# Kernel optimization log

Measured on AMD Instinct MI355X. Metric: run time of the kernel, lower is better.

## Reference

```python
import jax, jax.numpy as jnp
import numpy as np

# ---- column/activation layout (matches transformer_info init kwarg) ----
N_COLS = 20          # continuous data columns
MODES = 50           # VGM modes per column (gumbel-softmax width)
SPAN = MODES + 1     # 1 tanh scalar + MODES gumbel logits
IN_DIM = 2048
OUT_DIM = N_COLS * SPAN  # 1020
TAU = 0.2
B = 16384
EPS = 1e-9

_spans = []
for i in range(N_COLS):
    st = i * SPAN
    _spans.append((st, st + 1, 0))          # tanh span (alpha)
    _spans.append((st + 1, st + SPAN, 1))   # gumbel-softmax span (beta/d)
N_SEG = len(_spans)

_seg = np.zeros(OUT_DIM, np.int32)   # segment id per output feature
_typ = np.zeros(OUT_DIM, np.int32)   # 0 = tanh, 1 = gumbel-softmax
for si, (s, e, t) in enumerate(_spans):
    _seg[s:e] = si
    _typ[s:e] = t
SEG = jnp.asarray(_seg)
TYP = jnp.asarray(_typ)


def setup_inputs() -> dict:
    key = jax.random.key(0)
    kx, kw, kb, ku = jax.random.split(key, 4)
    bound = 1.0 / np.sqrt(IN_DIM)  # init_bounded(dim=input_dim)
    x = jax.random.normal(kx, (B, IN_DIM), dtype=jnp.float32)
    W = jax.random.uniform(kw, (IN_DIM, OUT_DIM), minval=-bound, maxval=bound, dtype=jnp.float32)
    b = jax.random.uniform(kb, (OUT_DIM,), minval=-bound, maxval=bound, dtype=jnp.float32)
    u = jax.random.uniform(ku, (B, OUT_DIM), dtype=jnp.float32)  # uniform driving gumbel noise
    return {"x": x, "W": W, "b": b, "u": u}


def _segment_softmax(z):
    # softmax over each transformer_info span, fused via segment ops.
    zT = z.T  # [D, B]
    m = jax.ops.segment_max(zT, SEG, num_segments=N_SEG)      # [S, B]
    e = jnp.exp(zT - m[SEG])
    s = jax.ops.segment_sum(e, SEG, num_segments=N_SEG)       # [S, B]
    return (e / s[SEG]).T  # [B, D]


def reference(x, W, b, u):
    outputs = x @ W + b  # [B, OUT_DIM]
    # Gumbel(0,1) noise from uniform u
    g = -jnp.log(-jnp.log(jnp.clip(u, EPS, 1.0 - EPS)))
    soft = _segment_softmax((outputs + g) / TAU)
    # type 0 -> tanh, type 1 -> gumbel-softmax (single fused select)
    data_t = jnp.where(TYP == 0, jnp.tanh(outputs), soft)
    return outputs, data_t
```

## Files before the change

### kernel.cpp

```cpp
#include <hip/hip_runtime.h>
#include <stdint.h>

#define MDIM 16384
#define NDIM 1020
#define KDIM 2048
#define NPAD 1024
#define TK   (KDIM / 64)

typedef __attribute__((ext_vector_type(4))) float f32x4;
typedef __attribute__((ext_vector_type(8))) short short8;

#define MFMA16(a, b, c) __builtin_amdgcn_mfma_f32_16x16x32_bf16((a), (b), (c), 0, 0, 0)

template <int OFF>
static __device__ __forceinline__ short8 dsr(unsigned addr) {
    short8 r;
    asm volatile("ds_read_b128 %0, %1 offset:%2" : "=v"(r) : "v"(addr), "i"(OFF));
    return r;
}
template <int OFF>
static __device__ __forceinline__ void dsw64(unsigned addr, uint2 v) {
    asm volatile("ds_write_b64 %0, %1 offset:%2" :: "v"(addr), "v"(v), "i"(OFF));
}

__device__ __forceinline__ unsigned packbf(float lo, float hi) {
    const unsigned r0 = __float_as_uint(lo) + 0x8000u;
    const unsigned r1 = __float_as_uint(hi) + 0x8000u;
    return __builtin_amdgcn_perm(r1, r0, 0x07060302u);
}

__device__ __forceinline__ unsigned short f2bf(float f) {
    unsigned int u = __float_as_uint(f);
    unsigned int r = (u + 0x7FFFu + ((u >> 16) & 1u)) >> 16;
    return (unsigned short)r;
}

__global__ void prep_w_kernel(const float* __restrict__ W,
                              unsigned short* __restrict__ Wt) {
    const int id = blockIdx.x * 256 + threadIdx.x;
    const int n0 = (id & 255) * 4;
    const int k0 = (id >> 8) * 4;
    float a[4][4];
    if (n0 < NDIM) {
#pragma unroll
        for (int i = 0; i < 4; ++i) {
            const float* p = W + (size_t)(k0 + i) * NDIM + n0;
            a[i][0] = p[0]; a[i][1] = p[1]; a[i][2] = p[2]; a[i][3] = p[3];
        }
    } else {
#pragma unroll
        for (int i = 0; i < 4; ++i)
#pragma unroll
            for (int j = 0; j < 4; ++j) a[i][j] = 0.f;
    }
#pragma unroll
    for (int j = 0; j < 4; ++j) {
        uint2 p;
        p.x = (unsigned)f2bf(a[0][j]) | ((unsigned)f2bf(a[1][j]) << 16);
        p.y = (unsigned)f2bf(a[2][j]) | ((unsigned)f2bf(a[3][j]) << 16);
        *(uint2*)(Wt + (size_t)(n0 + j) * KDIM + k0) = p;
    }
}

__global__ void prep_x_kernel(const float* __restrict__ x,
                              unsigned short* __restrict__ Xb) {
    const size_t total = (size_t)MDIM * KDIM;
    const size_t stride = (size_t)gridDim.x * 256 * 8;
    for (size_t i = ((size_t)blockIdx.x * 256 + threadIdx.x) * 8; i < total; i += stride) {
        const float4 v0 = *(const float4*)(x + i);
        const float4 v1 = *(const float4*)(x + i + 4);
        uint4 p;
        p.x = (unsigned)f2bf(v0.x) | ((unsigned)f2bf(v0.y) << 16);
        p.y = (unsigned)f2bf(v0.z) | ((unsigned)f2bf(v0.w) << 16);
        p.z = (unsigned)f2bf(v1.x) | ((unsigned)f2bf(v1.y) << 16);
        p.w = (unsigned)f2bf(v1.z) | ((unsigned)f2bf(v1.w) << 16);
        *(uint4*)(Xb + i) = p;
    }
}

extern "C" __global__ __launch_bounds__(512, 2) void gemm10_kernel(
    const float* __restrict__ x,
    const unsigned short* __restrict__ Wt,
    const float* __restrict__ bias,
    float* __restrict__ out) {
    extern __shared__ unsigned short lds_raw[];

    const int tid  = threadIdx.x;
    const int lane = tid & 63;
    const int wid  = tid >> 6;
    const int wr   = wid >> 2;
    const int wc   = wid & 3;

    const int bid = blockIdx.x;
    const int swz = (bid & 7) * 32 + (bid >> 3);
    const int bm  = swz >> 2;
    const int bn  = swz & 3;

    const int srow = wid * 8 + (lane >> 3);
    const int scb  = ((lane & 7) ^ (lane >> 3)) * 8;
    const unsigned short* bS = Wt + (size_t)(bn * 256 + srow) * KDIM + scb;

#define STAGEB(BUFI, STRIPE, S) do {                                             \
    const unsigned short* sp_ =                                                  \
        bS + (size_t)((STRIPE) * 64) * KDIM + (size_t)(((S) & 31) * 64);         \
    __builtin_amdgcn_global_load_lds(                                            \
        (const __attribute__((address_space(1))) unsigned int*)sp_,              \
        (__attribute__((address_space(3))) unsigned int*)(lds_raw +              \
            (BUFI) * 32768 + 16384 + ((STRIPE) * 64 + wid * 8) * 64),            \
        16, 0, 0);                                                               \
} while (0)

    const int h = lane >> 4, g = lane & 15;
    const float* aF = x + (size_t)(bm * 256 + wid * 32 + h) * KDIM + g * 4;

    const unsigned ldsbase =
        (unsigned)(uintptr_t)(__attribute__((address_space(3))) unsigned short*)lds_raw;
    const unsigned awbE =
        ldsbase + (unsigned)(wid * 32 + h) * 128 +
        ((unsigned)((g >> 1) ^ h) << 4) + (unsigned)(g & 1) * 8;
    const unsigned awbO  = awbE ^ 0x40u;
    const unsigned awb0E = awbE,           awb0O = awbO;
    const unsigned awb1E = awbE + 65536u,  awb1O = awbO + 65536u;

    float4 av[8];
#define AGLD(T) {                                                     \
    const float* ap_ = aF + (size_t)(((T) & 31) * 64);                \
    av[0] = *(const float4*)(ap_);                                    \
    av[1] = *(const float4*)(ap_ + 4 * KDIM);                         \
    av[2] = *(const float4*)(ap_ + 8 * KDIM);                         \
    av[3] = *(const float4*)(ap_ + 12 * KDIM);                        \
    av[4] = *(const float4*)(ap_ + 16 * KDIM);                        \
    av[5] = *(const float4*)(ap_ + 20 * KDIM);                        \
    av[6] = *(const float4*)(ap_ + 24 * KDIM);                        \
    av[7] = *(const float4*)(ap_ + 28 * KDIM);                        \
}
#define CVT1(AWE, AWO, I)                                             \
    { uint2 v_;                                                       \
      v_.x = packbf(av[I].x, av[I].y);                                \
      v_.y = packbf(av[I].z, av[I].w);                                \
      dsw64<(I) * 512>(((I) & 1) ? (AWO) : (AWE), v_); }
#define CVTW(AWE, AWO)                                                \
    CVT1(AWE, AWO, 0) CVT1(AWE, AWO, 1) CVT1(AWE, AWO, 2)             \
    CVT1(AWE, AWO, 3) CVT1(AWE, AWO, 4) CVT1(AWE, AWO, 5)             \
    CVT1(AWE, AWO, 6) CVT1(AWE, AWO, 7)

    const unsigned l15 = lane & 15, hi = lane >> 4, l7 = lane & 7;
    const unsigned c0 = (unsigned)((0 * 4 + hi) ^ l7) << 4;
    const unsigned c1 = (unsigned)((1 * 4 + hi) ^ l7) << 4;
    const unsigned pbA = ldsbase + (unsigned)(wr * 128 + l15) * 128;
    const unsigned pbB = ldsbase + 32768u + (unsigned)(wc * 64 + l15) * 128;
    const unsigned aA0_0 = pbA + c0,          aA0_1 = pbA + c1;
    const unsigned aA1_0 = pbA + 65536u + c0, aA1_1 = pbA + 65536u + c1;
    const unsigned bB0_0 = pbB + c0,          bB0_1 = pbB + c1;
    const unsigned bB1_0 = pbB + 65536u + c0, bB1_1 = pbB + 65536u + c1;

    f32x4 acc[8][4];
#pragma unroll
    for (int i = 0; i < 8; ++i)
#pragma unroll
        for (int j = 0; j < 4; ++j) {
            f32x4 z = {0.f, 0.f, 0.f, 0.f};
            acc[i][j] = z;
        }

#define PH_TAIL                                                       \
    __builtin_amdgcn_s_barrier();                                     \
    asm volatile("s_waitcnt lgkmcnt(0)" ::: "memory");                \
    __builtin_amdgcn_sched_barrier(0);                                \
    __builtin_amdgcn_s_setprio(1);

#define PH_MFMA(MF0)                                                  \
    _Pragma("unroll")                                                 \
    for (int nf = 0; nf < 4; ++nf) {                                  \
        acc[MF0][nf]     = MFMA16(af0[0], bfv[nf][0], acc[MF0][nf]);      \
        acc[MF0][nf]     = MFMA16(af0[1], bfv[nf][1], acc[MF0][nf]);      \
        acc[MF0 + 1][nf] = MFMA16(af1[0], bfv[nf][0], acc[MF0 + 1][nf]);  \
        acc[MF0 + 1][nf] = MFMA16(af1[1], bfv[nf][1], acc[MF0 + 1][nf]);  \
    }                                                                 \
    __builtin_amdgcn_sched_barrier(0);                                \
    __builtin_amdgcn_s_setprio(0);

#define RDA(BUF, MF0)                                                 \
    af0[0] = dsr<(MF0) * 2048>(aA##BUF##_0);                          \
    af0[1] = dsr<(MF0) * 2048>(aA##BUF##_1);                          \
    af1[0] = dsr<(MF0) * 2048 + 2048>(aA##BUF##_0);                   \
    af1[1] = dsr<(MF0) * 2048 + 2048>(aA##BUF##_1);

#define RDB(BUF, NF)                                                  \
    bfv[NF][0] = dsr<(NF) * 2048>(bB##BUF##_0);                       \
    bfv[NF][1] = dsr<(NF) * 2048>(bB##BUF##_1);

#define TILE(T, BUF, NB, AWE, AWO)                                              \
  {                                                                             \
    short8 bfv[4][2];                                                           \
    short8 af0[2], af1[2];                                                      \
              \
    RDB(BUF, 0) RDB(BUF, 1) RDB(BUF, 2) RDB(BUF, 3)                             \
    RDA(BUF, 0)                                                                 \
    AGLD((T) + 1)                                                               \
    PH_TAIL                                                                     \
    PH_MFMA(0)                                                                  \
    __builtin_amdgcn_s_barrier();                                               \
                                                         \
    RDA(BUF, 2)                                                                 \
    STAGEB(NB, 0, (T) + 1); STAGEB(NB, 1, (T) + 1);                             \
    PH_TAIL                                                                     \
    PH_MFMA(2)                                                                  \
    __builtin_amdgcn_s_barrier();                                               \
                                                         \
    RDA(BUF, 4)                                                                 \
    STAGEB(NB, 2, (T) + 1); STAGEB(NB, 3, (T) + 1);                             \
    PH_TAIL                                                                     \
    PH_MFMA(4)                                                                  \
    __builtin_amdgcn_s_barrier();                                               \
       \
    RDA(BUF, 6)                                                                 \
    CVTW(AWE, AWO)                                                              \
    PH_TAIL                                                                     \
    PH_MFMA(6)                                                                  \
    asm volatile("s_waitcnt vmcnt(0)" ::: "memory");                            \
    __builtin_amdgcn_sched_barrier(0);                                          \
    __builtin_amdgcn_s_barrier();                                               \
  }

    AGLD(0)
    STAGEB(0, 0, 0); STAGEB(0, 1, 0); STAGEB(0, 2, 0); STAGEB(0, 3, 0);
    CVTW(awb0E, awb0O)
    asm volatile("s_waitcnt lgkmcnt(0)" ::: "memory");
    __builtin_amdgcn_sched_barrier(0);
    asm volatile("s_waitcnt vmcnt(0)" ::: "memory");
    __builtin_amdgcn_sched_barrier(0);
    __builtin_amdgcn_s_barrier();

    for (int t2 = 0; t2 < TK; t2 += 2) {
        TILE(t2,     0, 1, awb1E, awb1O)
        TILE(t2 + 1, 1, 0, awb0E, awb0O)
    }

#pragma unroll
    for (int nf = 0; nf < 4; ++nf) {
        const int col = bn * 256 + wc * 64 + nf * 16 + (lane & 15);
        if (col < NDIM) {
            const float bv = bias[col];
#pragma unroll
            for (int mf = 0; mf < 8; ++mf) {
                const int row = bm * 256 + wr * 128 + mf * 16 + ((lane >> 4) << 2);
                float* op = out + (size_t)row * NDIM + col;
#pragma unroll
                for (int r = 0; r < 4; ++r)
                    op[(size_t)r * NDIM] = acc[mf][nf][r] + bv;
            }
        }
    }
#undef STAGEB
#undef AGLD
#undef CVT1
#undef CVTW
#undef PH_TAIL
#undef PH_MFMA
#undef RDA
#undef RDB
#undef TILE
}

__global__ void gemm_bf_kernel(const unsigned short* __restrict__ Xb,
                               const unsigned short* __restrict__ Wt,
                               const float* __restrict__ bias,
                               float* __restrict__ out) {
    __shared__ __align__(16) unsigned short As[128][32];
    __shared__ __align__(16) unsigned short Bs[128][32];

    const int tid  = threadIdx.x;
    const int lane = tid & 63;
    const int wid  = tid >> 6;
    const int wr   = wid >> 1;
    const int wc   = wid & 1;
    const int bn   = blockIdx.x;
    const int bm   = blockIdx.y;

    f32x4 acc[4][4];
#pragma unroll
    for (int i = 0; i < 4; ++i)
#pragma unroll
        for (int j = 0; j < 4; ++j) {
            f32x4 z = {0.f, 0.f, 0.f, 0.f};
            acc[i][j] = z;
        }

    const unsigned short* abase =
        Xb + (size_t)(bm * 128 + wid * 16 + (lane >> 2)) * KDIM + (lane & 3) * 8;
    const unsigned short* bbase =
        Wt + (size_t)(bn * 128 + wid * 16 + (lane >> 2)) * KDIM + (lane & 3) * 8;

    for (int kt = 0; kt < KDIM; kt += 32) {
#pragma unroll
        for (int j = 0; j < 2; ++j)
            __builtin_amdgcn_global_load_lds(
                (const __attribute__((address_space(1))) unsigned int*)(abase + (size_t)j * 64 * KDIM + kt),
                (__attribute__((address_space(3))) unsigned int*)(&As[j * 64 + wid * 16][0]),
                16, 0, 0);
#pragma unroll
        for (int j = 0; j < 2; ++j)
            __builtin_amdgcn_global_load_lds(
                (const __attribute__((address_space(1))) unsigned int*)(bbase + (size_t)j * 64 * KDIM + kt),
                (__attribute__((address_space(3))) unsigned int*)(&Bs[j * 64 + wid * 16][0]),
                16, 0, 0);
        __syncthreads();

        short8 af[4], bfr[4];
#pragma unroll
        for (int mi = 0; mi < 4; ++mi)
            af[mi] = *(const short8*)&As[wr * 64 + mi * 16 + (lane & 15)][(lane >> 4) * 8];
#pragma unroll
        for (int ni = 0; ni < 4; ++ni)
            bfr[ni] = *(const short8*)&Bs[wc * 64 + ni * 16 + (lane & 15)][(lane >> 4) * 8];

#pragma unroll
        for (int mi = 0; mi < 4; ++mi)
#pragma unroll
            for (int ni = 0; ni < 4; ++ni)
                acc[mi][ni] = MFMA16(af[mi], bfr[ni], acc[mi][ni]);

        __syncthreads();
    }

#pragma unroll
    for (int ni = 0; ni < 4; ++ni) {
        const int col = bn * 128 + wc * 64 + ni * 16 + (lane & 15);
        if (col < NDIM) {
            const float bv = bias[col];
#pragma unroll
            for (int mi = 0; mi < 4; ++mi) {
                const int row = bm * 128 + wr * 64 + mi * 16 + ((lane >> 4) << 2);
                float* op = out + (size_t)row * NDIM + col;
#pragma unroll
                for (int r = 0; r < 4; ++r)
                    op[(size_t)r * NDIM] = acc[mi][ni][r] + bv;
            }
        }
    }
}

__global__ void act_kernel(const float* __restrict__ outp,
                           const float* __restrict__ u,
                           float* __restrict__ dt) {
    const int lane  = threadIdx.x & 63;
    const int gwave = (blockIdx.x * 256 + threadIdx.x) >> 6;
    const int nwave = gridDim.x * 4;
    const int total = MDIM * 20;
    const float NEG_INF = -__builtin_inff();

    for (int unit = gwave; unit < total; unit += nwave) {
        const int row = unit / 20;
        const int sp  = unit - row * 20;
        const size_t base = (size_t)row * NDIM + sp * 51;

        float o = 0.f, uu = 0.5f;
        if (lane < 51) {
            o  = outp[base + lane];
            uu = u[base + lane];
        }
        const bool soft = (lane >= 1) && (lane < 51);

        const float uc = fmaxf(uu, 1e-9f);
        const float g  = -__logf(-__logf(uc));
        float z = soft ? (o + g) * 5.0f : NEG_INF;

        float m = z;
#pragma unroll
        for (int off = 32; off; off >>= 1) m = fmaxf(m, __shfl_xor(m, off));
        float e = soft ? __expf(z - m) : 0.f;
        float s = e;
#pragma unroll
        for (int off = 32; off; off >>= 1) s += __shfl_xor(s, off);

        float res;
        if (lane == 0) {
            const float ex = __expf(-2.0f * fabsf(o));
            const float t  = (1.0f - ex) / (1.0f + ex);
            res = copysignf(t, o);
        } else {
            res = e / s;
        }
        if (lane < 51) dt[base + lane] = res;
    }
}

extern "C" void kernel_launch(void* const* d_in, const int* in_sizes, int n_in,
                              void* d_out, int out_size, void* d_ws, size_t ws_size,
                              hipStream_t stream) {
    const float* x = (const float*)d_in[0];
    const float* W = (const float*)d_in[1];
    const float* b = (const float*)d_in[2];
    const float* u = (const float*)d_in[3];
    float* out = (float*)d_out;
    float* dt  = out + (size_t)MDIM * NDIM;
    unsigned short* Wt = (unsigned short*)d_ws;
    unsigned short* Xb = Wt + (size_t)NPAD * KDIM;

    prep_w_kernel<<<512, 256, 0, stream>>>(W, Wt);

    const hipError_t attr_ok = hipFuncSetAttribute(
        (const void*)gemm10_kernel, hipFuncAttributeMaxDynamicSharedMemorySize, 131072);
    if (attr_ok == hipSuccess) {
        gemm10_kernel<<<256, 512, 131072, stream>>>(x, Wt, b, out);
    } else {
        prep_x_kernel<<<2048, 256, 0, stream>>>(x, Xb);
        gemm_bf_kernel<<<dim3(8, 128), 256, 0, stream>>>(Xb, Wt, b, out);
    }

    act_kernel<<<8192, 256, 0, stream>>>(out, u, dt);
}
```

Measured before the change: 183.4 us.

## Split GEMM block work across 16 waves with 64x64 per-wave tiles

```diff
diff --git a/kernel.cpp b/kernel.cpp
--- a/kernel.cpp
+++ b/kernel.cpp
@@ -78,7 +78,7 @@
     }
 }
 
-extern "C" __global__ __launch_bounds__(512, 2) void gemm10_kernel(
+extern "C" __global__ __launch_bounds__(1024, 4) void gemm17_kernel(
     const float* __restrict__ x,
     const unsigned short* __restrict__ Wt,
     const float* __restrict__ bias,
@@ -102,37 +102,33 @@
 
 #define STAGEB(BUFI, STRIPE, S) do {                                             \
     const unsigned short* sp_ =                                                  \
-        bS + (size_t)((STRIPE) * 64) * KDIM + (size_t)(((S) & 31) * 64);         \
+        bS + (size_t)((STRIPE) * 128) * KDIM + (size_t)(((S) & 31) * 64);        \
     __builtin_amdgcn_global_load_lds(                                            \
         (const __attribute__((address_space(1))) unsigned int*)sp_,              \
         (__attribute__((address_space(3))) unsigned int*)(lds_raw +              \
-            (BUFI) * 32768 + 16384 + ((STRIPE) * 64 + wid * 8) * 64),            \
+            (BUFI) * 32768 + 16384 + ((STRIPE) * 128 + wid * 8) * 64),           \
         16, 0, 0);                                                               \
 } while (0)
 
     const int h = lane >> 4, g = lane & 15;
-    const float* aF = x + (size_t)(bm * 256 + wid * 32 + h) * KDIM + g * 4;
+    const float* aF = x + (size_t)(bm * 256 + wid * 16 + h) * KDIM + g * 4;
 
     const unsigned ldsbase =
         (unsigned)(uintptr_t)(__attribute__((address_space(3))) unsigned short*)lds_raw;
     const unsigned awbE =
-        ldsbase + (unsigned)(wid * 32 + h) * 128 +
+        ldsbase + (unsigned)(wid * 16 + h) * 128 +
         ((unsigned)((g >> 1) ^ h) << 4) + (unsigned)(g & 1) * 8;
     const unsigned awbO  = awbE ^ 0x40u;
     const unsigned awb0E = awbE,           awb0O = awbO;
     const unsigned awb1E = awbE + 65536u,  awb1O = awbO + 65536u;
 
-    float4 av[8];
+    float4 av[4];
 #define AGLD(T) {                                                     \
     const float* ap_ = aF + (size_t)(((T) & 31) * 64);                \
     av[0] = *(const float4*)(ap_);                                    \
     av[1] = *(const float4*)(ap_ + 4 * KDIM);                         \
     av[2] = *(const float4*)(ap_ + 8 * KDIM);                         \
     av[3] = *(const float4*)(ap_ + 12 * KDIM);                        \
-    av[4] = *(const float4*)(ap_ + 16 * KDIM);                        \
-    av[5] = *(const float4*)(ap_ + 20 * KDIM);                        \
-    av[6] = *(const float4*)(ap_ + 24 * KDIM);                        \
-    av[7] = *(const float4*)(ap_ + 28 * KDIM);                        \
 }
 #define CVT1(AWE, AWO, I)                                             \
     { uint2 v_;                                                       \
@@ -140,23 +136,21 @@
       v_.y = packbf(av[I].z, av[I].w);                                \
       dsw64<(I) * 512>(((I) & 1) ? (AWO) : (AWE), v_); }
 #define CVTW(AWE, AWO)                                                \
-    CVT1(AWE, AWO, 0) CVT1(AWE, AWO, 1) CVT1(AWE, AWO, 2)             \
-    CVT1(AWE, AWO, 3) CVT1(AWE, AWO, 4) CVT1(AWE, AWO, 5)             \
-    CVT1(AWE, AWO, 6) CVT1(AWE, AWO, 7)
+    CVT1(AWE, AWO, 0) CVT1(AWE, AWO, 1) CVT1(AWE, AWO, 2) CVT1(AWE, AWO, 3)
 
     const unsigned l15 = lane & 15, hi = lane >> 4, l7 = lane & 7;
     const unsigned c0 = (unsigned)((0 * 4 + hi) ^ l7) << 4;
     const unsigned c1 = (unsigned)((1 * 4 + hi) ^ l7) << 4;
-    const unsigned pbA = ldsbase + (unsigned)(wr * 128 + l15) * 128;
+    const unsigned pbA = ldsbase + (unsigned)(wr * 64 + l15) * 128;
     const unsigned pbB = ldsbase + 32768u + (unsigned)(wc * 64 + l15) * 128;
     const unsigned aA0_0 = pbA + c0,          aA0_1 = pbA + c1;
     const unsigned aA1_0 = pbA + 65536u + c0, aA1_1 = pbA + 65536u + c1;
     const unsigned bB0_0 = pbB + c0,          bB0_1 = pbB + c1;
     const unsigned bB1_0 = pbB + 65536u + c0, bB1_1 = pbB + 65536u + c1;
 
-    f32x4 acc[8][4];
-#pragma unroll
-    for (int i = 0; i < 8; ++i)
+    f32x4 acc[4][4];
+#pragma unroll
+    for (int i = 0; i < 4; ++i)
 #pragma unroll
         for (int j = 0; j < 4; ++j) {
             f32x4 z = {0.f, 0.f, 0.f, 0.f};
@@ -169,62 +163,43 @@
     __builtin_amdgcn_sched_barrier(0);                                \
     __builtin_amdgcn_s_setprio(1);
 
-#define PH_MFMA(MF0)                                                  \
+#define PH_MFMA                                                       \
     _Pragma("unroll")                                                 \
-    for (int nf = 0; nf < 4; ++nf) {                                  \
-        acc[MF0][nf]     = MFMA16(af0[0], bfv[nf][0], acc[MF0][nf]);      \
-        acc[MF0][nf]     = MFMA16(af0[1], bfv[nf][1], acc[MF0][nf]);      \
-        acc[MF0 + 1][nf] = MFMA16(af1[0], bfv[nf][0], acc[MF0 + 1][nf]);  \
-        acc[MF0 + 1][nf] = MFMA16(af1[1], bfv[nf][1], acc[MF0 + 1][nf]);  \
-    }                                                                 \
+    for (int nf = 0; nf < 4; ++nf)                                    \
+        _Pragma("unroll")                                             \
+        for (int mf = 0; mf < 4; ++mf)                                \
+            acc[mf][nf] = MFMA16(af[mf], bfv[nf], acc[mf][nf]);       \
     __builtin_amdgcn_sched_barrier(0);                                \
     __builtin_amdgcn_s_setprio(0);
 
-#define RDA(BUF, MF0)                                                 \
-    af0[0] = dsr<(MF0) * 2048>(aA##BUF##_0);                          \
-    af0[1] = dsr<(MF0) * 2048>(aA##BUF##_1);                          \
-    af1[0] = dsr<(MF0) * 2048 + 2048>(aA##BUF##_0);                   \
-    af1[1] = dsr<(MF0) * 2048 + 2048>(aA##BUF##_1);
-
-#define RDB(BUF, NF)                                                  \
-    bfv[NF][0] = dsr<(NF) * 2048>(bB##BUF##_0);                       \
-    bfv[NF][1] = dsr<(NF) * 2048>(bB##BUF##_1);
+#define RD8(ABASE, BBASE)                                             \
+    af[0]  = dsr<0>(ABASE);    af[1]  = dsr<2048>(ABASE);             \
+    af[2]  = dsr<4096>(ABASE); af[3]  = dsr<6144>(ABASE);             \
+    bfv[0] = dsr<0>(BBASE);    bfv[1] = dsr<2048>(BBASE);             \
+    bfv[2] = dsr<4096>(BBASE); bfv[3] = dsr<6144>(BBASE);
 
 #define TILE(T, BUF, NB, AWE, AWO)                                              \
   {                                                                             \
-    short8 bfv[4][2];                                                           \
-    short8 af0[2], af1[2];                                                      \
-              \
-    RDB(BUF, 0) RDB(BUF, 1) RDB(BUF, 2) RDB(BUF, 3)                             \
-    RDA(BUF, 0)                                                                 \
+    short8 af[4], bfv[4];                                                       \
+                      \
+    RD8(aA##BUF##_0, bB##BUF##_0)                                               \
+    STAGEB(NB, 0, (T) + 1); STAGEB(NB, 1, (T) + 1);                             \
     AGLD((T) + 1)                                                               \
     PH_TAIL                                                                     \
-    PH_MFMA(0)                                                                  \
+    PH_MFMA                                                                     \
     __builtin_amdgcn_s_barrier();                                               \
-                                                         \
-    RDA(BUF, 2)                                                                 \
-    STAGEB(NB, 0, (T) + 1); STAGEB(NB, 1, (T) + 1);                             \
-    PH_TAIL                                                                     \
-    PH_MFMA(2)                                                                  \
-    __builtin_amdgcn_s_barrier();                                               \
-                                                         \
-    RDA(BUF, 4)                                                                 \
-    STAGEB(NB, 2, (T) + 1); STAGEB(NB, 3, (T) + 1);                             \
-    PH_TAIL                                                                     \
-    PH_MFMA(4)                                                                  \
-    __builtin_amdgcn_s_barrier();                                               \
-       \
-    RDA(BUF, 6)                                                                 \
+           \
+    RD8(aA##BUF##_1, bB##BUF##_1)                                               \
     CVTW(AWE, AWO)                                                              \
     PH_TAIL                                                                     \
-    PH_MFMA(6)                                                                  \
+    PH_MFMA                                                                     \
     asm volatile("s_waitcnt vmcnt(0)" ::: "memory");                            \
     __builtin_amdgcn_sched_barrier(0);                                          \
     __builtin_amdgcn_s_barrier();                                               \
   }
 
     AGLD(0)
-    STAGEB(0, 0, 0); STAGEB(0, 1, 0); STAGEB(0, 2, 0); STAGEB(0, 3, 0);
+    STAGEB(0, 0, 0); STAGEB(0, 1, 0);
     CVTW(awb0E, awb0O)
     asm volatile("s_waitcnt lgkmcnt(0)" ::: "memory");
     __builtin_amdgcn_sched_barrier(0);
@@ -243,8 +218,8 @@
         if (col < NDIM) {
             const float bv = bias[col];
 #pragma unroll
-            for (int mf = 0; mf < 8; ++mf) {
-                const int row = bm * 256 + wr * 128 + mf * 16 + ((lane >> 4) << 2);
+            for (int mf = 0; mf < 4; ++mf) {
+                const int row = bm * 256 + wr * 64 + mf * 16 + ((lane >> 4) << 2);
                 float* op = out + (size_t)row * NDIM + col;
 #pragma unroll
                 for (int r = 0; r < 4; ++r)
@@ -258,8 +233,7 @@
 #undef CVTW
 #undef PH_TAIL
 #undef PH_MFMA
-#undef RDA
-#undef RDB
+#undef RD8
 #undef TILE
 }
 
@@ -401,9 +375,9 @@
     prep_w_kernel<<<512, 256, 0, stream>>>(W, Wt);
 
     const hipError_t attr_ok = hipFuncSetAttribute(
-        (const void*)gemm10_kernel, hipFuncAttributeMaxDynamicSharedMemorySize, 131072);
+        (const void*)gemm17_kernel, hipFuncAttributeMaxDynamicSharedMemorySize, 131072);
     if (attr_ok == hipSuccess) {
-        gemm10_kernel<<<256, 512, 131072, stream>>>(x, Wt, b, out);
+        gemm17_kernel<<<256, 1024, 131072, stream>>>(x, Wt, b, out);
     } else {
         prep_x_kernel<<<2048, 256, 0, stream>>>(x, Xb);
         gemm_bf_kernel<<<dim3(8, 128), 256, 0, stream>>>(Xb, Wt, b, out);
```

Result: slower. 213.5 us (+16.4%).
